# Kernel optimization log

Measured on AMD Instinct MI355X. Metric: run time of the kernel, lower is better.

## Reference

```python
import jax, jax.numpy as jnp
import numpy as np

N_NODES = 50000
N_EDGES = 600000
IN_DIM = 9
HID = 128
OUT_DIM = 6


def _mlp2(x, W1, b1, W2, b2):
    # Linear -> ReLU -> Linear
    h = jax.nn.relu(x @ W1 + b1)
    return h @ W2 + b2


def setup_inputs() -> dict:
    key = jax.random.key(0)
    ks = jax.random.split(key, 16)

    def lin(k, fan_in, fan_out):
        # torch nn.Linear default init: U(-1/sqrt(fan_in), 1/sqrt(fan_in))
        bound = 1.0 / np.sqrt(fan_in)
        kw, kb = jax.random.split(k)
        W = jax.random.uniform(kw, (fan_in, fan_out), jnp.float32, -bound, bound)
        b = jax.random.uniform(kb, (fan_out,), jnp.float32, -bound, bound)
        return W, b

    node_states = jax.random.normal(ks[0], (N_NODES, IN_DIM), jnp.float32)
    edge_index = jax.random.randint(ks[1], (2, N_EDGES), 0, N_NODES, jnp.int64 if jax.config.jax_enable_x64 else jnp.int32)
    edge_attr = jax.random.uniform(ks[2], (N_EDGES, 1), jnp.float32)

    ne_W1, ne_b1 = lin(ks[3], IN_DIM, HID)
    ne_W2, ne_b2 = lin(ks[4], HID, HID)
    ee_W1, ee_b1 = lin(ks[5], 2 * HID + 1, HID)
    ee_W2, ee_b2 = lin(ks[6], HID, HID)
    nu_W1, nu_b1 = lin(ks[7], 2 * HID, HID)
    nu_W2, nu_b2 = lin(ks[8], HID, OUT_DIM)

    return {
        "node_states": node_states, "edge_index": edge_index, "edge_attr": edge_attr,
        "ne_W1": ne_W1, "ne_b1": ne_b1, "ne_W2": ne_W2, "ne_b2": ne_b2,
        "ee_W1": ee_W1, "ee_b1": ee_b1, "ee_W2": ee_W2, "ee_b2": ee_b2,
        "nu_W1": nu_W1, "nu_b1": nu_b1, "nu_W2": nu_W2, "nu_b2": nu_b2,
    }


def reference(node_states, edge_index, edge_attr,
              ne_W1, ne_b1, ne_W2, ne_b2,
              ee_W1, ee_b1, ee_W2, ee_b2,
              nu_W1, nu_b1, nu_W2, nu_b2):
    num_nodes = node_states.shape[0]
    # node encoder: [N, 9] -> [N, 128]
    h_v = _mlp2(node_states, ne_W1, ne_b1, ne_W2, ne_b2)

    row, col = edge_index[0], edge_index[1]
    # gather endpoints + concat edge features: [E, 257]
    edge_inputs = jnp.concatenate([h_v[row], h_v[col], edge_attr], axis=1)
    h_e = _mlp2(edge_inputs, ee_W1, ee_b1, ee_W2, ee_b2)  # [E, 128]

    # scatter-add messages to destination nodes (index_add_ on col)
    agg_messages = jax.ops.segment_sum(h_e, col, num_segments=num_nodes)  # [N, 128]

    node_inputs = jnp.concatenate([h_v, agg_messages], axis=1)  # [N, 256]
    gnn_deltas = _mlp2(node_inputs, nu_W1, nu_b1, nu_W2, nu_b2)  # [N, 6]
    return gnn_deltas
```

## Files before the change

kernel.cpp:

```cpp
#include <hip/hip_runtime.h>

#define N_NODES 50000
#define N_EDGES 600000
#define IN_DIM 9
#define HID 128
#define OUT_DIM 6
#define SCAN_BLKS ((N_NODES + 255) / 256)

typedef __attribute__((ext_vector_type(8))) short short8;
typedef __attribute__((ext_vector_type(4))) float f32x4;

__device__ __forceinline__ void split_bf16(float x, ushort& hi, ushort& lo) {
    unsigned u = __float_as_uint(x);
    unsigned r = u + 0x7FFF + ((u >> 16) & 1);
    hi = (ushort)(r >> 16);
    float hif = __uint_as_float((unsigned)hi << 16);
    lo = (ushort)(__float_as_uint(x - hif) >> 16);
}

__global__ __launch_bounds__(128)
void node_encoder(const float* __restrict__ x,
                  const float* __restrict__ W1, const float* __restrict__ b1,
                  const float* __restrict__ W2, const float* __restrict__ b2,
                  float* __restrict__ hv)
{
    const int t  = threadIdx.x;
    const int n0 = blockIdx.x * 4;

    __shared__ float xs[4][12];
    __shared__ float h1[4][132];

    if (t < 4 * IN_DIM) {
        int n = t / IN_DIM, k = t % IN_DIM;
        xs[n][k] = x[(n0 + n) * IN_DIM + k];
    }
    __syncthreads();

    float w[IN_DIM];
#pragma unroll
    for (int k = 0; k < IN_DIM; ++k) w[k] = W1[k * HID + t];
    const float bb1 = b1[t];
#pragma unroll
    for (int n = 0; n < 4; ++n) {
        float s = bb1;
#pragma unroll
        for (int k = 0; k < IN_DIM; ++k) s += xs[n][k] * w[k];
        h1[n][t] = fmaxf(s, 0.f);
    }
    __syncthreads();

    float acc[4] = {0.f, 0.f, 0.f, 0.f};
    for (int k = 0; k < HID; k += 4) {
        const float w0 = W2[(k + 0) * HID + t];
        const float w1 = W2[(k + 1) * HID + t];
        const float w2 = W2[(k + 2) * HID + t];
        const float w3 = W2[(k + 3) * HID + t];
#pragma unroll
        for (int n = 0; n < 4; ++n) {
            const float4 a = *(const float4*)&h1[n][k];
            acc[n] += a.x * w0 + a.y * w1 + a.z * w2 + a.w * w3;
        }
    }
    const float bb2 = b2[t];
#pragma unroll
    for (int n = 0; n < 4; ++n)
        hv[(size_t)(n0 + n) * HID + t] = acc[n] + bb2;
}

__global__ __launch_bounds__(256)
void csr_count(const int* __restrict__ col, int* __restrict__ cnt) {
    const int i = blockIdx.x * 256 + threadIdx.x;
    if (i < N_EDGES) atomicAdd(&cnt[col[i]], 1);
}

__global__ __launch_bounds__(256)
void scan_part(const int* __restrict__ cnt, int* __restrict__ part) {
    __shared__ int s[256];
    const int tid = threadIdx.x;
    const int i = blockIdx.x * 256 + tid;
    s[tid] = (i < N_NODES) ? cnt[i] : 0;
    __syncthreads();
#pragma unroll
    for (int off = 128; off > 0; off >>= 1) {
        if (tid < off) s[tid] += s[tid + off];
        __syncthreads();
    }
    if (tid == 0) part[blockIdx.x] = s[0];
}

__global__ __launch_bounds__(256)
void scan_scan(int* __restrict__ part) {
    __shared__ int s[256];
    const int tid = threadIdx.x;
    const int v = (tid < SCAN_BLKS) ? part[tid] : 0;
    s[tid] = v;
    __syncthreads();
    for (int off = 1; off < 256; off <<= 1) {
        int x = (tid >= off) ? s[tid - off] : 0;
        __syncthreads();
        s[tid] += x;
        __syncthreads();
    }
    part[tid] = s[tid] - v;
}

__global__ __launch_bounds__(256)
void scan_final(const int* __restrict__ cnt, const int* __restrict__ part,
                int* __restrict__ ofs, int* __restrict__ cursor) {
    __shared__ int s[256];
    const int tid = threadIdx.x;
    const int i = blockIdx.x * 256 + tid;
    const int v = (i < N_NODES) ? cnt[i] : 0;
    s[tid] = v;
    __syncthreads();
    for (int off = 1; off < 256; off <<= 1) {
        int x = (tid >= off) ? s[tid - off] : 0;
        __syncthreads();
        s[tid] += x;
        __syncthreads();
    }
    const int excl = part[blockIdx.x] + s[tid] - v;
    if (i <= N_NODES) ofs[i] = excl;
    if (i <  N_NODES) cursor[i] = excl;
}

__global__ __launch_bounds__(256)
void csr_fill(const int* __restrict__ col, int* __restrict__ cursor,
              int* __restrict__ eid) {
    const int i = blockIdx.x * 256 + threadIdx.x;
    if (i < N_EDGES) {
        const int p = atomicAdd(&cursor[col[i]], 1);
        eid[p] = i;
    }
}

__global__ __launch_bounds__(64)
void pack_weights(const float* __restrict__ W1, const float* __restrict__ W2,
                  ushort* __restrict__ p1h, ushort* __restrict__ p1l,
                  ushort* __restrict__ p2h, ushort* __restrict__ p2l)
{
    const int l = threadIdx.x;
    const int b = blockIdx.x;
    if (b < 64) {
        const int kt = b >> 3, nt = b & 7;
        const int kbase = kt * 32 + 8 * (l >> 4);
        const int n = nt * 16 + (l & 15);
#pragma unroll
        for (int j = 0; j < 8; ++j) {
            ushort hi, lo;
            split_bf16(W1[(kbase + j) * HID + n], hi, lo);
            p1h[(b * 64 + l) * 8 + j] = hi;
            p1l[(b * 64 + l) * 8 + j] = lo;
        }
    } else {
        const int u = b - 64;
        const int kt = u >> 3, nt = u & 7;
        const int kbase = kt * 32 + 8 * (l >> 4);
        const int n = nt * 16 + (l & 15);
#pragma unroll
        for (int j = 0; j < 8; ++j) {
            ushort hi, lo;
            split_bf16(W2[(kbase + j) * HID + n], hi, lo);
            p2h[(u * 64 + l) * 8 + j] = hi;
            p2l[(u * 64 + l) * 8 + j] = lo;
        }
    }
}

__global__ __launch_bounds__(256, 4)
void edge_mfma(const float* __restrict__ hv,
               const int* __restrict__ row, const int* __restrict__ col,
               const float* __restrict__ eattr,
               const int* __restrict__ eids,
               const ushort* __restrict__ p1h, const ushort* __restrict__ p1l,
               const ushort* __restrict__ p2h, const ushort* __restrict__ p2l,
               const float* __restrict__ W1,
               const float* __restrict__ b1, const float* __restrict__ b2,
               float* __restrict__ agg)
{
    __shared__ __align__(16) ushort AB[16384];
    __shared__ int   rows_s[32], cols_s[32];
    __shared__ float attr_s[32];

    const int tid = threadIdx.x;
    const int e0  = blockIdx.x * 32;

    if (tid < 32) {
        const int e = eids[e0 + tid];
        rows_s[tid] = row[e];
        cols_s[tid] = col[e];
        attr_s[tid] = eattr[e];
    }
    __syncthreads();

#pragma unroll
    for (int c = tid; c < 1024; c += 256) {
        const int kt   = c >> 7;
        const int rem  = c & 127;
        const int hh   = rem >> 6;
        const int lane = rem & 63;
        const int edge = hh * 16 + (lane & 15);
        const int kk   = kt * 32 + 8 * (lane >> 4);
        const int node = (kk < 128) ? rows_s[edge] : cols_s[edge];
        const float* src = &hv[(size_t)node * HID + (kk & 127)];
        short8 vh, vl;
#pragma unroll
        for (int j = 0; j < 8; ++j) {
            ushort h_, l_;
            split_bf16(src[j], h_, l_);
            vh[j] = (short)h_; vl[j] = (short)l_;
        }
        *(short8*)&AB[c * 8]        = vh;
        *(short8*)&AB[8192 + c * 8] = vl;
    }
    __syncthreads();

    const int l  = tid & 63;
    const int w  = tid >> 6;
    const int h  = w & 1;
    const int nh = w >> 1;
    const int gl = l >> 4;
    const int r  = l & 15;

    f32x4 acc[4] = {{0,0,0,0},{0,0,0,0},{0,0,0,0},{0,0,0,0}};
    for (int kt = 0; kt < 8; ++kt) {
        const short8 ah = *(const short8*)&AB[((kt * 2 + h) * 64 + l) * 8];
        const short8 al = *(const short8*)&AB[8192 + ((kt * 2 + h) * 64 + l) * 8];
#pragma unroll
        for (int i = 0; i < 4; ++i) {
            const int nt = nh * 4 + i;
            const short8 bh = *(const short8*)&p1h[((kt * 8 + nt) * 64 + l) * 8];
            const short8 bl = *(const short8*)&p1l[((kt * 8 + nt) * 64 + l) * 8];
            acc[i] = __builtin_amdgcn_mfma_f32_16x16x32_bf16(ah, bh, acc[i], 0, 0, 0);
            acc[i] = __builtin_amdgcn_mfma_f32_16x16x32_bf16(ah, bl, acc[i], 0, 0, 0);
            acc[i] = __builtin_amdgcn_mfma_f32_16x16x32_bf16(al, bh, acc[i], 0, 0, 0);
        }
    }
    __syncthreads();

#pragma unroll
    for (int i = 0; i < 4; ++i) {
        const int ncol = nh * 64 + i * 16 + r;
        const float w256 = W1[256 * HID + ncol];
        const float bb   = b1[ncol];
        const int kt2 = ncol >> 5;
        const int g2  = (ncol >> 3) & 3;
        const int j   = ncol & 7;
#pragma unroll
        for (int q = 0; q < 4; ++q) {
            const int er = gl * 4 + q;
            const float a = attr_s[h * 16 + er];
            float v = fmaxf(acc[i][q] + bb + a * w256, 0.f);
            ushort hi, lo;
            split_bf16(v, hi, lo);
            const int cell = (kt2 * 2 + h) * 64 + g2 * 16 + er;
            AB[cell * 8 + j]        = hi;
            AB[4096 + cell * 8 + j] = lo;
        }
    }
    __syncthreads();

    f32x4 acc2[4] = {{0,0,0,0},{0,0,0,0},{0,0,0,0},{0,0,0,0}};
    for (int kt = 0; kt < 4; ++kt) {
        const short8 ah = *(const short8*)&AB[((kt * 2 + h) * 64 + l) * 8];
        const short8 al = *(const short8*)&AB[4096 + ((kt * 2 + h) * 64 + l) * 8];
#pragma unroll
        for (int i = 0; i < 4; ++i) {
            const int nt = nh * 4 + i;
            const short8 bh = *(const short8*)&p2h[((kt * 8 + nt) * 64 + l) * 8];
            const short8 bl = *(const short8*)&p2l[((kt * 8 + nt) * 64 + l) * 8];
            acc2[i] = __builtin_amdgcn_mfma_f32_16x16x32_bf16(ah, bh, acc2[i], 0, 0, 0);
            acc2[i] = __builtin_amdgcn_mfma_f32_16x16x32_bf16(ah, bl, acc2[i], 0, 0, 0);
            acc2[i] = __builtin_amdgcn_mfma_f32_16x16x32_bf16(al, bh, acc2[i], 0, 0, 0);
        }
    }

    const int er0 = h * 16 + gl * 4;
    const int n0s = cols_s[er0 + 0];
    const int n1s = cols_s[er0 + 1];
    const int n2s = cols_s[er0 + 2];
    const int n3s = cols_s[er0 + 3];
#pragma unroll
    for (int i = 0; i < 4; ++i) {
        const int ncol = nh * 64 + i * 16 + r;
        const float bb = b2[ncol];
        const float v0 = acc2[i][0] + bb;
        const float v1 = acc2[i][1] + bb;
        const float v2 = acc2[i][2] + bb;
        const float v3 = acc2[i][3] + bb;
        if (n0s == n3s) {
            atomicAdd(&agg[(size_t)n0s * HID + ncol], v0 + v1 + v2 + v3);
        } else {
            atomicAdd(&agg[(size_t)n0s * HID + ncol], v0);
            atomicAdd(&agg[(size_t)n1s * HID + ncol], v1);
            atomicAdd(&agg[(size_t)n2s * HID + ncol], v2);
            atomicAdd(&agg[(size_t)n3s * HID + ncol], v3);
        }
    }
}

__global__ __launch_bounds__(128)
void node_update(const float* __restrict__ hv,
                 const float* __restrict__ agg,
                 const float* __restrict__ W1, const float* __restrict__ b1,
                 const float* __restrict__ W2, const float* __restrict__ b2,
                 float* __restrict__ out)
{
    const int t  = threadIdx.x;
    const int n0 = blockIdx.x * 4;

    __shared__ float ins[4][260];
    __shared__ float h1[4][132];
    __shared__ float part[4][2][6];

#pragma unroll
    for (int n = 0; n < 4; ++n) {
        ins[n][t]       = hv[(size_t)(n0 + n) * HID + t];
        ins[n][HID + t] = agg[(size_t)(n0 + n) * HID + t];
    }
    __syncthreads();

    float acc[4] = {0.f, 0.f, 0.f, 0.f};
    for (int k = 0; k < 2 * HID; k += 4) {
        const float w0 = W1[(k + 0) * HID + t];
        const float w1 = W1[(k + 1) * HID + t];
        const float w2 = W1[(k + 2) * HID + t];
        const float w3 = W1[(k + 3) * HID + t];
#pragma unroll
        for (int n = 0; n < 4; ++n) {
            const float4 a = *(const float4*)&ins[n][k];
            acc[n] += a.x * w0 + a.y * w1 + a.z * w2 + a.w * w3;
        }
    }
    const float bb1 = b1[t];
#pragma unroll
    for (int n = 0; n < 4; ++n) h1[n][t] = fmaxf(acc[n] + bb1, 0.f);
    __syncthreads();

    float wv[6];
#pragma unroll
    for (int j = 0; j < 6; ++j) wv[j] = W2[t * OUT_DIM + j];

#pragma unroll
    for (int n = 0; n < 4; ++n) {
        const float v = h1[n][t];
        float p[6];
#pragma unroll
        for (int j = 0; j < 6; ++j) p[j] = v * wv[j];
#pragma unroll
        for (int off = 32; off > 0; off >>= 1) {
#pragma unroll
            for (int j = 0; j < 6; ++j) p[j] += __shfl_down(p[j], off);
        }
        if ((t & 63) == 0) {
#pragma unroll
            for (int j = 0; j < 6; ++j) part[n][t >> 6][j] = p[j];
        }
    }
    __syncthreads();

    if (t < 24) {
        const int n = t / 6, j = t % 6;
        out[(size_t)(n0 + n) * OUT_DIM + j] = part[n][0][j] + part[n][1][j] + b2[j];
    }
}

extern "C" void kernel_launch(void* const* d_in, const int* in_sizes, int n_in,
                              void* d_out, int out_size, void* d_ws, size_t ws_size,
                              hipStream_t stream) {
    const float* node_states = (const float*)d_in[0];
    const int*   edge_index  = (const int*)d_in[1];
    const float* edge_attr   = (const float*)d_in[2];
    const float* ne_W1 = (const float*)d_in[3];
    const float* ne_b1 = (const float*)d_in[4];
    const float* ne_W2 = (const float*)d_in[5];
    const float* ne_b2 = (const float*)d_in[6];
    const float* ee_W1 = (const float*)d_in[7];
    const float* ee_b1 = (const float*)d_in[8];
    const float* ee_W2 = (const float*)d_in[9];
    const float* ee_b2 = (const float*)d_in[10];
    const float* nu_W1 = (const float*)d_in[11];
    const float* nu_b1 = (const float*)d_in[12];
    const float* nu_W2 = (const float*)d_in[13];
    const float* nu_b2 = (const float*)d_in[14];

    const int* row = edge_index;
    const int* col = edge_index + N_EDGES;

    float* hv     = (float*)d_ws;
    float* agg    = hv + (size_t)N_NODES * HID;
    int*   cnt    = (int*)(agg + (size_t)N_NODES * HID);
    int*   ofs    = cnt + N_NODES;
    int*   cursor = ofs + (N_NODES + 1);
    int*   partb  = cursor + N_NODES;
    int*   eids   = partb + 256;
    ushort* p1h   = (ushort*)(((uintptr_t)(eids + N_EDGES) + 15) & ~(uintptr_t)15);
    ushort* p1l   = p1h + 32768;
    ushort* p2h   = p1l + 32768;
    ushort* p2l   = p2h + 16384;

    hipMemsetAsync(agg, 0, (size_t)N_NODES * HID * sizeof(float), stream);
    hipMemsetAsync(cnt, 0, N_NODES * sizeof(int), stream);

    node_encoder<<<N_NODES / 4, 128, 0, stream>>>(
        node_states, ne_W1, ne_b1, ne_W2, ne_b2, hv);

    csr_count<<<(N_EDGES + 255) / 256, 256, 0, stream>>>(col, cnt);
    scan_part<<<SCAN_BLKS, 256, 0, stream>>>(cnt, partb);
    scan_scan<<<1, 256, 0, stream>>>(partb);
    scan_final<<<SCAN_BLKS, 256, 0, stream>>>(cnt, partb, ofs, cursor);
    csr_fill<<<(N_EDGES + 255) / 256, 256, 0, stream>>>(col, cursor, eids);

    pack_weights<<<96, 64, 0, stream>>>(ee_W1, ee_W2, p1h, p1l, p2h, p2l);

    edge_mfma<<<N_EDGES / 32, 256, 0, stream>>>(
        hv, row, col, edge_attr, eids,
        p1h, p1l, p2h, p2l, ee_W1, ee_b1, ee_b2, agg);

    node_update<<<N_NODES / 4, 128, 0, stream>>>(
        hv, agg, nu_W1, nu_b1, nu_W2, nu_b2, (float*)d_out);
}
```

Measured before the change: 721.2 us.

## Store node embeddings pre-split as bf16 hi/lo and load MFMA operands directly

The node encoder now writes its output as separate bf16 high and low planes instead of fp32, so the edge kernel no longer re-splits each gathered row per edge. The edge kernel drops the LDS staging pass and one barrier, loading A-fragments for the first GEMM straight from global memory in MFMA layout. The smaller LDS footprint lets the occupancy hint rise to 8 blocks per CU. Node update rebuilds fp32 from hi+lo, which loses a few low mantissa bits relative to the original fp32 values.

```diff
diff --git a/kernel.cpp b/kernel.cpp
--- a/kernel.cpp
+++ b/kernel.cpp
@@ -22,7 +22,7 @@
 void node_encoder(const float* __restrict__ x,
                   const float* __restrict__ W1, const float* __restrict__ b1,
                   const float* __restrict__ W2, const float* __restrict__ b2,
-                  float* __restrict__ hv)
+                  ushort* __restrict__ hvh, ushort* __restrict__ hvl)
 {
     const int t  = threadIdx.x;
     const int n0 = blockIdx.x * 4;
@@ -63,8 +63,12 @@
     }
     const float bb2 = b2[t];
 #pragma unroll
-    for (int n = 0; n < 4; ++n)
-        hv[(size_t)(n0 + n) * HID + t] = acc[n] + bb2;
+    for (int n = 0; n < 4; ++n) {
+        ushort hi, lo;
+        split_bf16(acc[n] + bb2, hi, lo);
+        hvh[(size_t)(n0 + n) * HID + t] = hi;
+        hvl[(size_t)(n0 + n) * HID + t] = lo;
+    }
 }
 
 __global__ __launch_bounds__(256)
@@ -167,8 +171,8 @@
     }
 }
 
-__global__ __launch_bounds__(256, 4)
-void edge_mfma(const float* __restrict__ hv,
+__global__ __launch_bounds__(256, 8)
+void edge_mfma(const ushort* __restrict__ hvh, const ushort* __restrict__ hvl,
                const int* __restrict__ row, const int* __restrict__ col,
                const float* __restrict__ eattr,
                const int* __restrict__ eids,
@@ -178,7 +182,8 @@
                const float* __restrict__ b1, const float* __restrict__ b2,
                float* __restrict__ agg)
 {
-    __shared__ __align__(16) ushort AB[16384];
+    __shared__ __align__(16) ushort H1h[4096];
+    __shared__ __align__(16) ushort H1l[4096];
     __shared__ int   rows_s[32], cols_s[32];
     __shared__ float attr_s[32];
 
@@ -190,28 +195,6 @@
         rows_s[tid] = row[e];
         cols_s[tid] = col[e];
         attr_s[tid] = eattr[e];
-    }
-    __syncthreads();
-
-#pragma unroll
-    for (int c = tid; c < 1024; c += 256) {
-        const int kt   = c >> 7;
-        const int rem  = c & 127;
-        const int hh   = rem >> 6;
-        const int lane = rem & 63;
-        const int edge = hh * 16 + (lane & 15);
-        const int kk   = kt * 32 + 8 * (lane >> 4);
-        const int node = (kk < 128) ? rows_s[edge] : cols_s[edge];
-        const float* src = &hv[(size_t)node * HID + (kk & 127)];
-        short8 vh, vl;
-#pragma unroll
-        for (int j = 0; j < 8; ++j) {
-            ushort h_, l_;
-            split_bf16(src[j], h_, l_);
-            vh[j] = (short)h_; vl[j] = (short)l_;
-        }
-        *(short8*)&AB[c * 8]        = vh;
-        *(short8*)&AB[8192 + c * 8] = vl;
     }
     __syncthreads();
 
@@ -222,10 +205,16 @@
     const int gl = l >> 4;
     const int r  = l & 15;
 
+    const int edge  = h * 16 + r;
+    const int rbyte = rows_s[edge] * 256 + gl * 16;
+    const int cbyte = cols_s[edge] * 256 + gl * 16;
+
     f32x4 acc[4] = {{0,0,0,0},{0,0,0,0},{0,0,0,0},{0,0,0,0}};
+#pragma unroll
     for (int kt = 0; kt < 8; ++kt) {
-        const short8 ah = *(const short8*)&AB[((kt * 2 + h) * 64 + l) * 8];
-        const short8 al = *(const short8*)&AB[8192 + ((kt * 2 + h) * 64 + l) * 8];
+        const int off = (kt < 4) ? (rbyte + kt * 64) : (cbyte + (kt - 4) * 64);
+        const short8 ah = *(const short8*)((const char*)hvh + off);
+        const short8 al = *(const short8*)((const char*)hvl + off);
 #pragma unroll
         for (int i = 0; i < 4; ++i) {
             const int nt = nh * 4 + i;
@@ -236,7 +225,6 @@
             acc[i] = __builtin_amdgcn_mfma_f32_16x16x32_bf16(al, bh, acc[i], 0, 0, 0);
         }
     }
-    __syncthreads();
 
 #pragma unroll
     for (int i = 0; i < 4; ++i) {
@@ -254,16 +242,17 @@
             ushort hi, lo;
             split_bf16(v, hi, lo);
             const int cell = (kt2 * 2 + h) * 64 + g2 * 16 + er;
-            AB[cell * 8 + j]        = hi;
-            AB[4096 + cell * 8 + j] = lo;
+            H1h[cell * 8 + j] = hi;
+            H1l[cell * 8 + j] = lo;
         }
     }
     __syncthreads();
 
     f32x4 acc2[4] = {{0,0,0,0},{0,0,0,0},{0,0,0,0},{0,0,0,0}};
+#pragma unroll
     for (int kt = 0; kt < 4; ++kt) {
-        const short8 ah = *(const short8*)&AB[((kt * 2 + h) * 64 + l) * 8];
-        const short8 al = *(const short8*)&AB[4096 + ((kt * 2 + h) * 64 + l) * 8];
+        const short8 ah = *(const short8*)&H1h[((kt * 2 + h) * 64 + l) * 8];
+        const short8 al = *(const short8*)&H1l[((kt * 2 + h) * 64 + l) * 8];
 #pragma unroll
         for (int i = 0; i < 4; ++i) {
             const int nt = nh * 4 + i;
@@ -300,7 +289,7 @@
 }
 
 __global__ __launch_bounds__(128)
-void node_update(const float* __restrict__ hv,
+void node_update(const ushort* __restrict__ hvh, const ushort* __restrict__ hvl,
                  const float* __restrict__ agg,
                  const float* __restrict__ W1, const float* __restrict__ b1,
                  const float* __restrict__ W2, const float* __restrict__ b2,
@@ -315,7 +304,9 @@
 
 #pragma unroll
     for (int n = 0; n < 4; ++n) {
-        ins[n][t]       = hv[(size_t)(n0 + n) * HID + t];
+        const unsigned hh = hvh[(size_t)(n0 + n) * HID + t];
+        const unsigned ll = hvl[(size_t)(n0 + n) * HID + t];
+        ins[n][t]       = __uint_as_float(hh << 16) + __uint_as_float(ll << 16);
         ins[n][HID + t] = agg[(size_t)(n0 + n) * HID + t];
     }
     __syncthreads();
@@ -387,8 +378,9 @@
     const int* row = edge_index;
     const int* col = edge_index + N_EDGES;
 
-    float* hv     = (float*)d_ws;
-    float* agg    = hv + (size_t)N_NODES * HID;
+    ushort* hvh   = (ushort*)d_ws;
+    ushort* hvl   = hvh + (size_t)N_NODES * HID;
+    float*  agg   = (float*)(hvl + (size_t)N_NODES * HID);
     int*   cnt    = (int*)(agg + (size_t)N_NODES * HID);
     int*   ofs    = cnt + N_NODES;
     int*   cursor = ofs + (N_NODES + 1);
@@ -403,7 +395,7 @@
     hipMemsetAsync(cnt, 0, N_NODES * sizeof(int), stream);
 
     node_encoder<<<N_NODES / 4, 128, 0, stream>>>(
-        node_states, ne_W1, ne_b1, ne_W2, ne_b2, hv);
+        node_states, ne_W1, ne_b1, ne_W2, ne_b2, hvh, hvl);
 
     csr_count<<<(N_EDGES + 255) / 256, 256, 0, stream>>>(col, cnt);
     scan_part<<<SCAN_BLKS, 256, 0, stream>>>(cnt, partb);
@@ -414,9 +406,9 @@
     pack_weights<<<96, 64, 0, stream>>>(ee_W1, ee_W2, p1h, p1l, p2h, p2l);
 
     edge_mfma<<<N_EDGES / 32, 256, 0, stream>>>(
-        hv, row, col, edge_attr, eids,
+        hvh, hvl, row, col, edge_attr, eids,
         p1h, p1l, p2h, p2l, ee_W1, ee_b1, ee_b2, agg);
 
     node_update<<<N_NODES / 4, 128, 0, stream>>>(
-        hv, agg, nu_W1, nu_b1, nu_W2, nu_b2, (float*)d_out);
-}
+        hvh, hvl, agg, nu_W1, nu_b1, nu_W2, nu_b2, (float*)d_out);
+}
```

New measurement: 699.4 us. 3.0% less time.
